# Performance work log

Hardware: AMD Instinct MI355X
Metric: run time of the kernel (lower is better)

## Reference

```python
import jax, jax.numpy as jnp
import numpy as np
import math

# ----- sizes -----
NUM_EDGES = 16384
NUM_NODES = 1024          # senders index into [0, NUM_NODES)
N_MUL = 64                # multiplicity n = V.shape[1]
AVG_NEIGH = 16.0          # avg_num_neighbors
F_IN = 64                 # scalar feature dim of x

# ----- real spherical harmonics (component normalization: sum_m Y_lm^2 = 2l+1) -----
_S3 = math.sqrt(3.0); _S5 = math.sqrt(5.0); _S15 = math.sqrt(15.0)
_C33 = math.sqrt(70.0)/4.0; _C32 = math.sqrt(105.0)/2.0
_C31 = math.sqrt(42.0)/4.0; _C30 = math.sqrt(7.0)/2.0; _CXYZ = math.sqrt(105.0)

def _sph(vn):
    x, y, z = vn[:, 0], vn[:, 1], vn[:, 2]
    Y0 = jnp.ones_like(x)[:, None]
    Y1 = _S3 * vn
    Y2 = jnp.stack([_S15*x*y, _S15*y*z, 0.5*_S5*(3*z*z - 1), _S15*x*z, 0.5*_S15*(x*x - y*y)], axis=1)
    Y3 = jnp.stack([_C33*y*(3*x*x - y*y), _CXYZ*x*y*z, _C31*y*(5*z*z - 1), _C30*z*(5*z*z - 3), _C31*x*(5*z*z - 1), _C32*z*(x*x - y*y), _C33*x*(x*x - 3*y*y)], axis=1)
    return [Y0, Y1, Y2, Y3]

# monomial form of the same SH, used to derive EXACT Clebsch-Gordan coefficients
_SHP = {
    0: [[(1.0, (0,0,0))]],
    1: [[(_S3, (1,0,0))], [(_S3, (0,1,0))], [(_S3, (0,0,1))]],
    2: [[(_S15, (1,1,0))], [(_S15, (0,1,1))], [(1.5*_S5, (0,0,2)), (-0.5*_S5, (0,0,0))], [(_S15, (1,0,1))], [(0.5*_S15, (2,0,0)), (-0.5*_S15, (0,2,0))]],
    3: [[(3*_C33, (2,1,0)), (-_C33, (0,3,0))], [(_CXYZ, (1,1,1))], [(5*_C31, (0,1,2)), (-_C31, (0,1,0))], [(5*_C30, (0,0,3)), (-3*_C30, (0,0,1))], [(5*_C31, (1,0,2)), (-_C31, (1,0,0))], [(_C32, (2,0,1)), (-_C32, (0,2,1))], [(_C33, (3,0,0)), (-3*_C33, (1,2,0))]],
}

def _dfact(n):
    r = 1
    while n > 1:
        r *= n; n -= 2
    return r

def _mono_int(e):
    # exact integral of x^a y^b z^c over the unit sphere
    a, b, c = e
    if (a % 2) or (b % 2) or (c % 2):
        return 0.0
    return 4.0*math.pi*_dfact(a-1)*_dfact(b-1)*_dfact(c-1)/_dfact(a+b+c+1)

def _pmul(p, q):
    return [(cp*cq, (a1+a2, b1+b2, c1+c2)) for cp, (a1,b1,c1) in p for cq, (a2,b2,c2) in q]

def _pint(p):
    return sum(c*_mono_int(e) for c, e in p)

def _cg(l1, l2, l3):
    # unique SO(3) intertwiner in this real-SH basis, scaled like e3nn component norm: sqrt(2l3+1)*w3j
    C = np.zeros((2*l1+1, 2*l2+1, 2*l3+1))
    for i, p1 in enumerate(_SHP[l1]):
        for j, p2 in enumerate(_SHP[l2]):
            p12 = _pmul(p1, p2)
            for k, p3 in enumerate(_SHP[l3]):
                C[i, j, k] = _pint(_pmul(p12, p3)) / (4.0*math.pi)
    return jnp.asarray(C / np.linalg.norm(C) * np.sqrt(2*l3+1), dtype=jnp.float32)

# tensor-product paths surviving filter_ir_out = 0e + 1o + 2e (inputs: SH 0e+1o+2e+3o, V 0e+1o+2e)
_PATHS0 = [(0,0), (1,1), (2,2)]
_PATHS1 = [(0,1), (1,0), (1,2), (2,1), (3,2)]
_PATHS2 = [(0,2), (1,1), (2,0), (2,2), (3,1)]
CGS = {(l1, l2, l3): _cg(l1, l2, l3) for l3, ps in ((0, _PATHS0), (1, _PATHS1), (2, _PATHS2)) for l1, l2 in ps}

# e3nn normalize_function(silu): divide by sqrt(E_{z~N(0,1)}[silu(z)^2])
_zg = np.linspace(-12.0, 12.0, 200001)
_phi = np.exp(-0.5*_zg*_zg)/np.sqrt(2.0*np.pi)
_sl = _zg/(1.0 + np.exp(-_zg))
ACT_C = float(np.sqrt(np.sum(_sl*_sl*_phi)*(_zg[1]-_zg[0])))

def _nsilu(v):
    return jax.nn.silu(v) / ACT_C

def _forward(vectors, x, V, senders, W_w, W1, W2, W3, Wv1, Wv2):
    E, n = V.shape[0], V.shape[1]
    d = jnp.linalg.norm(vectors, axis=1, keepdims=True)                 # [E,1] edge lengths
    vn = vectors / d
    Y = jnp.concatenate(_sph(vn), axis=1)                               # [E,16], ell = 0..3
    w = (x @ W_w) / math.sqrt(x.shape[1])                               # [E,n] edge weights (1-layer MLP, no act)
    wY = w[:, :, None] * Y[:, None, :]                                  # [E,n,16]
    agg = jax.ops.segment_sum(wY, senders, num_segments=NUM_NODES)[senders]  # scatter_sum + map_back
    agg = agg / math.sqrt(AVG_NEIGH)
    A = jnp.split(agg, [1, 4, 9], axis=2)                               # SH chunks: dims 1,3,5,7
    B = jnp.split(V, [1, 4], axis=2)                                    # V chunks: dims 1,3,5
    def tp(l1, l2, l3):
        return jnp.einsum('eni,enj,ijk->enk', A[l1], B[l2], CGS[(l1, l2, l3)])
    scal = jnp.concatenate([tp(a, b, 0) for a, b in _PATHS0], axis=2)   # [E,n,3] new scalars
    V1 = jnp.concatenate([tp(a, b, 1) for a, b in _PATHS1], axis=1)     # [E,5n,3] 1o paths
    V2 = jnp.concatenate([tp(a, b, 2) for a, b in _PATHS2], axis=1)     # [E,5n,5] 2e paths
    h = jnp.concatenate([x, scal.reshape(E, 3*n)], axis=1)              # [E, F_IN+3n]
    h = _nsilu(h @ W1 / math.sqrt(h.shape[1]))
    h = _nsilu(h @ W2 / math.sqrt(W2.shape[0]))
    h = h @ W3 / math.sqrt(W3.shape[0])                                 # output_activation=False
    # poly_envelope(p-1=5, 2), p=6: 1 - 28 d^6 + 48 d^7 - 21 d^8 on [0,1), 0 outside
    u = 1.0 - 28.0*d**6 + 48.0*d**7 - 21.0*d**8
    x_out = jnp.where(d < 1.0, u, 0.0) * h                              # [E,64]
    o1 = jnp.einsum('emi,mo->eoi', V1, Wv1) / math.sqrt(V1.shape[1])    # Linear per irrep: [E,n,3]
    o2 = jnp.einsum('emi,mo->eoi', V2, Wv2) / math.sqrt(V2.shape[1])    # [E,n,5]
    # output 0e block has no input path -> zeros (e3nn Linear, no bias)
    V_out = jnp.concatenate([jnp.zeros((E, n, 1), x_out.dtype), o1, o2], axis=2)  # [E,n,9]
    return x_out, V_out

def setup_inputs():
    key = jax.random.key(0)
    ks = jax.random.split(key, 10)
    E = NUM_EDGES
    vectors = 0.35 * jax.random.normal(ks[0], (E, 3), jnp.float32)   # mostly inside cutoff radius 1
    x = jax.random.normal(ks[1], (E, F_IN), jnp.float32)
    V = jax.random.normal(ks[2], (E, N_MUL, 9), jnp.float32)
    senders = jax.random.randint(ks[3], (E,), 0, NUM_NODES, dtype=jnp.int32)
    W_w = jax.random.normal(ks[4], (F_IN, N_MUL), jnp.float32)
    W1 = jax.random.normal(ks[5], (F_IN + 3*N_MUL, 64), jnp.float32)
    W2 = jax.random.normal(ks[6], (64, 64), jnp.float32)
    W3 = jax.random.normal(ks[7], (64, 64), jnp.float32)
    Wv1 = jax.random.normal(ks[8], (5*N_MUL, N_MUL), jnp.float32)
    Wv2 = jax.random.normal(ks[9], (5*N_MUL, N_MUL), jnp.float32)
    return {"vectors": vectors, "x": x, "V": V, "senders": senders, "W_w": W_w, "W1": W1, "W2": W2, "W3": W3, "Wv1": Wv1, "Wv2": Wv2}

def reference(vectors, x, V, senders, W_w, W1, W2, W3, Wv1, Wv2):
    return _forward(vectors, x, V, senders, W_w, W1, W2, W3, Wv1, Wv2)
```

## Files before the change

kernel.cpp:

```cpp
#include <hip/hip_runtime.h>
#include <math.h>

#define NNODES 1024
#define EDGES 16384
#define EB 4

typedef __attribute__((ext_vector_type(8))) short short8;
typedef __attribute__((ext_vector_type(4))) float f32x4;

__device__ __forceinline__ unsigned short f2bf(float f) {
  union { float f; unsigned int u; } v; v.f = f;
  unsigned int r = v.u + 0x7fffu + ((v.u >> 16) & 1u);
  return (unsigned short)(r >> 16);
}

__device__ __constant__ int PL1[13] = {0,1,2, 0,1,1,2,3, 0,1,2,2,3};
__device__ __constant__ int PL2[13] = {0,1,2, 1,0,2,1,2, 2,1,0,2,1};
__device__ __constant__ int PL3[13] = {0,0,0, 1,1,1,1,1, 2,2,2,2,2};
__device__ __constant__ int PCG[13] = {0,1,10, 35,44,53,98,143, 248,273,318,343,468};

__device__ __constant__ double SHC[16][2] = {
  {1.0, 0.0},
  {1.7320508075688772, 0.0},
  {1.7320508075688772, 0.0},
  {1.7320508075688772, 0.0},
  {3.8729833462074170, 0.0},
  {3.8729833462074170, 0.0},
  {3.3541019662496844, -1.1180339887498949},
  {3.8729833462074170, 0.0},
  {1.9364916731037085, -1.9364916731037085},
  {6.2749501990055667, -2.0916500663351889},
  {10.246950765959598, 0.0},
  {8.1009258730098255, -1.6201851746019651},
  {6.6143782776614768, -3.9686269665968861},
  {8.1009258730098255, -1.6201851746019651},
  {5.1234753829797990, -5.1234753829797990},
  {2.0916500663351889, -6.2749501990055667},
};
__device__ __constant__ int SHE[16][2] = {
  {0,0},{1,0},{16,0},{256,0},
  {17,0},{272,0},{512,0},{257,0},{2,32},
  {18,48},{273,0},{528,16},{768,256},{513,1},{258,288},{3,33}};

__global__ __launch_bounds__(256) void prep(
    const float* __restrict__ Wv1, const float* __restrict__ Wv2,
    const float* __restrict__ W1, const float* __restrict__ W2, const float* __restrict__ W3,
    unsigned short* __restrict__ wv1f, unsigned short* __restrict__ wv2f,
    unsigned short* __restrict__ w1f, unsigned short* __restrict__ w2f,
    unsigned short* __restrict__ w3f,
    float* __restrict__ cg, float* __restrict__ actp, int* __restrict__ counts)
{
  const int bid = blockIdx.x;
  const int t = threadIdx.x;

  if (bid < 13) {
    if (bid < 4) counts[bid*256 + t] = 0;
    __shared__ double sh[256];
    const int p = bid;
    const int LOFF[4] = {0,1,4,9};
    int l1 = PL1[p], l2 = PL2[p], l3 = PL3[p];
    int n1 = 2*l1+1, n2 = 2*l2+1, n3 = 2*l3+1;
    int nent = n1*n2*n3;
    const unsigned long long DP =
        1ULL | (1ULL<<7) | (1ULL<<14) | (2ULL<<21) | (3ULL<<28)
      | (8ULL<<35) | (15ULL<<42) | (48ULL<<49) | (105ULL<<56);
    double v = 0.0;
    if (t < nent) {
      int i = t / (n2*n3);
      int rem = t - i*(n2*n3);
      int j = rem / n3;
      int k = rem - j*n3;
      int lm1 = LOFF[l1]+i, lm2 = LOFF[l2]+j, lm3 = LOFF[l3]+k;
      double cs1[2] = {SHC[lm1][0], SHC[lm1][1]}; int es1[2] = {SHE[lm1][0], SHE[lm1][1]};
      double cs2[2] = {SHC[lm2][0], SHC[lm2][1]}; int es2[2] = {SHE[lm2][0], SHE[lm2][1]};
      double cs3[2] = {SHC[lm3][0], SHC[lm3][1]}; int es3[2] = {SHE[lm3][0], SHE[lm3][1]};
      #pragma unroll
      for (int t1 = 0; t1 < 2; t1++)
      #pragma unroll
      for (int t2 = 0; t2 < 2; t2++)
      #pragma unroll
      for (int t3 = 0; t3 < 2; t3++) {
        double cc = cs1[t1]*cs2[t2]*cs3[t3];
        int s = es1[t1] + es2[t2] + es3[t3];
        int a = s & 15, b = (s >> 4) & 15, c = (s >> 8) & 15;
        if (!((a|b|c) & 1)) {
          double num = (double)(int)((DP >> (7*a)) & 127)
                     * (double)(int)((DP >> (7*b)) & 127)
                     * (double)(int)((DP >> (7*c)) & 127);
          double den = (double)(int)((DP >> (7*(a+b+c+2))) & 127);
          v += cc * (num / den);
        }
      }
    }
    sh[t] = (t < nent) ? v*v : 0.0;
    __syncthreads();
    for (int d = 128; d > 0; d >>= 1) {
      if (t < d) sh[t] += sh[t+d];
      __syncthreads();
    }
    double scale = sqrt((double)(2*l3+1)) / sqrt(sh[0]);
    if (t < nent) cg[PCG[p] + t] = (float)(v * scale);

  } else if (bid < 21) {
    __shared__ float shf[256];
    const int b = bid - 13;
    const float dz = 24.0f / 200000.0f;
    float s = 0.f;
    for (int i = b*256 + t; i <= 200000; i += 8*256) {
      float z = -12.0f + dz * (float)i;
      float ph = __expf(-0.5f * z * z) * 0.3989422804014327f;
      float sl = z / (1.f + __expf(-z));
      s = fmaf(sl*sl, ph, s);
    }
    shf[t] = s;
    __syncthreads();
    for (int d = 128; d > 0; d >>= 1) {
      if (t < d) shf[t] += shf[t + d];
      __syncthreads();
    }
    if (t == 0) actp[b] = shf[0];

  } else {
    const int wid = t >> 6, lane = t & 63;
    const int g = (bid - 21)*4 + wid;
    const float* src; unsigned short* dst; int nk, f;
    if (g < 40)       { src = Wv1; dst = wv1f; nk = 10; f = g; }
    else if (g < 80)  { src = Wv2; dst = wv2f; nk = 10; f = g - 40; }
    else if (g < 112) { src = W1;  dst = w1f;  nk = 8;  f = g - 80; }
    else if (g < 120) { src = W2;  dst = w2f;  nk = 2;  f = g - 112; }
    else              { src = W3;  dst = w3f;  nk = 2;  f = g - 120; }
    int nt = f / nk;
    int ks = f - nt*nk;
    unsigned short us[8];
    #pragma unroll
    for (int j = 0; j < 8; j++) {
      float v = src[(ks*32 + (lane>>4)*8 + j)*64 + nt*16 + (lane & 15)];
      us[j] = f2bf(v);
    }
    uint4 pk;
    pk.x = (unsigned)us[0] | ((unsigned)us[1] << 16);
    pk.y = (unsigned)us[2] | ((unsigned)us[3] << 16);
    pk.z = (unsigned)us[4] | ((unsigned)us[5] << 16);
    pk.w = (unsigned)us[6] | ((unsigned)us[7] << 16);
    *(uint4*)(dst + ((size_t)f*64 + lane)*8) = pk;
  }
}

__global__ __launch_bounds__(256) void edgepass(
    const float* __restrict__ x, const float* __restrict__ Ww,
    const int* __restrict__ senders,
    float* __restrict__ w_ws, int* __restrict__ counts, int* __restrict__ elist, int E)
{
  const int wid = threadIdx.x >> 6, lane = threadIdx.x & 63;
  const int e = blockIdx.x * 4 + wid;
  if (e >= E) return;
  float xv = x[e*64 + lane];
  float w = 0.f;
  #pragma unroll
  for (int f = 0; f < 64; f++)
    w = fmaf(__shfl(xv, f), Ww[f*64 + lane], w);
  w_ws[e*64 + lane] = w * 0.125f;
  if (lane == 0) {
    int s = senders[e];
    int pos = atomicAdd(&counts[s], 1) & 63;
    elist[s*64 + pos] = e;
  }
}

__global__ __launch_bounds__(256) void k_node(
    const float* __restrict__ vec, const float* __restrict__ w_ws,
    const int* __restrict__ counts, const int* __restrict__ elist,
    float* __restrict__ node_agg)
{
  __shared__ float red[4*1024];
  const int wid = threadIdx.x >> 6, lane = threadIdx.x & 63;
  const int s = blockIdx.x;
  const int deg = min(counts[s], 64);

  const float S3 = 1.7320508075688772f, S5 = 2.23606797749979f, S15 = 3.872983346207417f;
  const float C33 = 2.091650066335189f, C32 = 5.123475382979799f, C31 = 1.6201851746019651f;
  const float C30 = 1.3228756555322954f, CX = 10.246950765959598f;

  float A[16];
  #pragma unroll
  for (int k = 0; k < 16; k++) A[k] = 0.f;

  for (int ii = wid; ii < deg; ii += 4) {
    int e = elist[s*64 + ii];
    float vx = vec[e*3+0], vy = vec[e*3+1], vz = vec[e*3+2];
    float d = sqrtf(vx*vx + vy*vy + vz*vz);
    float X = vx/d, Yv = vy/d, Z = vz/d;
    float y[16];
    y[0] = 1.f;
    y[1] = S3*X;  y[2] = S3*Yv;  y[3] = S3*Z;
    y[4] = S15*X*Yv; y[5] = S15*Yv*Z; y[6] = 0.5f*S5*(3.f*Z*Z - 1.f);
    y[7] = S15*X*Z;  y[8] = 0.5f*S15*(X*X - Yv*Yv);
    y[9]  = C33*Yv*(3.f*X*X - Yv*Yv);
    y[10] = CX*X*Yv*Z;
    y[11] = C31*Yv*(5.f*Z*Z - 1.f);
    y[12] = C30*Z*(5.f*Z*Z - 3.f);
    y[13] = C31*X*(5.f*Z*Z - 1.f);
    y[14] = C32*Z*(X*X - Yv*Yv);
    y[15] = C33*X*(X*X - 3.f*Yv*Yv);
    float wv = w_ws[e*64 + lane];
    #pragma unroll
    for (int k = 0; k < 16; k++) A[k] = fmaf(wv, y[k], A[k]);
  }
  #pragma unroll
  for (int k = 0; k < 16; k++) red[wid*1024 + lane*16 + k] = A[k];
  __syncthreads();
  const int t = threadIdx.x;
  f32x4 v0 = ((f32x4*)red)[t];
  f32x4 v1 = ((f32x4*)red)[256 + t];
  f32x4 v2 = ((f32x4*)red)[512 + t];
  f32x4 v3 = ((f32x4*)red)[768 + t];
  f32x4 sum = v0 + v1 + v2 + v3;
  ((f32x4*)(node_agg + (size_t)s*1024))[t] = sum;
}

template<int L1, int L2, int L3>
__device__ __forceinline__ void tp_path(const float* __restrict__ cgp,
    const float a[16], const float b[9], float o[2*L3+1])
{
  constexpr int N1 = 2*L1+1, N2 = 2*L2+1, N3 = 2*L3+1;
  constexpr int AO = (L1==0) ? 0 : (L1==1) ? 1 : (L1==2) ? 4 : 9;
  constexpr int BO = (L2==0) ? 0 : (L2==1) ? 1 : 4;
  constexpr int LM1 = (L1==0) ? 0 : (L1==1) ? 1 : (L1==2) ? 4 : 9;
  constexpr int LM2 = (L2==0) ? 0 : (L2==1) ? 1 : 4;
  constexpr int LM3 = (L3==0) ? 0 : (L3==1) ? 1 : 4;
  static constexpr unsigned char PAR[16] =
      {0, 1,2,4, 3,6,0,5,0, 2,7,2,4,1,4,1};
  #pragma unroll
  for (int k = 0; k < N3; k++) o[k] = 0.f;
  int ci = 0;
  #pragma unroll
  for (int i = 0; i < N1; i++) {
    #pragma unroll
    for (int j = 0; j < N2; j++) {
      float ab = a[AO+i] * b[BO+j];
      #pragma unroll
      for (int k = 0; k < N3; k++) {
        if ((PAR[LM1+i] ^ PAR[LM2+j] ^ PAR[LM3+k]) == 0)
          o[k] = fmaf(ab, cgp[ci], o[k]);
        ci++;
      }
    }
  }
}

__global__ __launch_bounds__(256, 4) void edge_main(
    const float* __restrict__ vec, const float* __restrict__ x,
    const float* __restrict__ V, const int* __restrict__ senders,
    const float* __restrict__ node_agg, const float* __restrict__ cg,
    const unsigned short* __restrict__ wv1f, const unsigned short* __restrict__ wv2f,
    const unsigned short* __restrict__ w1f, const unsigned short* __restrict__ w2f,
    const unsigned short* __restrict__ w3f,
    float* __restrict__ out, int E, const float* __restrict__ actp)
{
  __shared__ __align__(16) unsigned short V1sh[12*328];
  __shared__ __align__(16) unsigned short V2sh[20*328];
  __shared__ __align__(16) unsigned short zrow[336];
  __shared__ __align__(16) unsigned short hsh[4*264];
  __shared__ __align__(16) unsigned short h1sh[4*72];
  __shared__ __align__(16) unsigned short h2sh[4*72];
  __shared__ __align__(16) float vosh[4*584];
  __shared__ float ush[EB];

  const int t = threadIdx.x;
  const int wid = t >> 6, lane = t & 63;
  const int e0 = blockIdx.x * EB;
  const size_t E64 = (size_t)E * 64;
  const float inv_actc = 1.f / sqrtf((actp[0]+actp[1]+actp[2]+actp[3]
                                     +actp[4]+actp[5]+actp[6]+actp[7]) * (24.0f/200000.0f));

  if (t < 168) ((unsigned int*)zrow)[t] = 0u;

  { int el = t >> 6, o = t & 63;
    hsh[el*264 + o] = f2bf(x[(e0+el)*64 + o]); }

  {
    const int eloc = wid;
    const int eg = e0 + eloc;
    const int s = senders[eg];

    float a[16];
    const float* nap = node_agg + s*1024 + lane*16;
    #pragma unroll
    for (int k = 0; k < 16; k++) a[k] = nap[k] * 0.25f;

    float b[9];
    const float* vp = V + (size_t)eg*576 + lane*9;
    #pragma unroll
    for (int j = 0; j < 9; j++) b[j] = vp[j];

    float o1[1], o3[3], o5[5];
    tp_path<0,0,0>(cg + 0,  a, b, o1); hsh[eloc*264 + 64 + lane*3 + 0] = f2bf(o1[0]);
    tp_path<1,1,0>(cg + 1,  a, b, o1); hsh[eloc*264 + 64 + lane*3 + 1] = f2bf(o1[0]);
    tp_path<2,2,0>(cg + 10, a, b, o1); hsh[eloc*264 + 64 + lane*3 + 2] = f2bf(o1[0]);
    tp_path<0,1,1>(cg + 35, a, b, o3);
    { int r = eloc*3; for (int i=0;i<3;i++) V1sh[(r+i)*328 + 0*64 + lane] = f2bf(o3[i]); }
    tp_path<1,0,1>(cg + 44, a, b, o3);
    { int r = eloc*3; for (int i=0;i<3;i++) V1sh[(r+i)*328 + 1*64 + lane] = f2bf(o3[i]); }
    tp_path<1,2,1>(cg + 53, a, b, o3);
    { int r = eloc*3; for (int i=0;i<3;i++) V1sh[(r+i)*328 + 2*64 + lane] = f2bf(o3[i]); }
    tp_path<2,1,1>(cg + 98, a, b, o3);
    { int r = eloc*3; for (int i=0;i<3;i++) V1sh[(r+i)*328 + 3*64 + lane] = f2bf(o3[i]); }
    tp_path<3,2,1>(cg + 143, a, b, o3);
    { int r = eloc*3; for (int i=0;i<3;i++) V1sh[(r+i)*328 + 4*64 + lane] = f2bf(o3[i]); }
    tp_path<0,2,2>(cg + 248, a, b, o5);
    { int r = eloc*5; for (int i=0;i<5;i++) V2sh[(r+i)*328 + 0*64 + lane] = f2bf(o5[i]); }
    tp_path<1,1,2>(cg + 273, a, b, o5);
    { int r = eloc*5; for (int i=0;i<5;i++) V2sh[(r+i)*328 + 1*64 + lane] = f2bf(o5[i]); }
    tp_path<2,0,2>(cg + 318, a, b, o5);
    { int r = eloc*5; for (int i=0;i<5;i++) V2sh[(r+i)*328 + 2*64 + lane] = f2bf(o5[i]); }
    tp_path<2,2,2>(cg + 343, a, b, o5);
    { int r = eloc*5; for (int i=0;i<5;i++) V2sh[(r+i)*328 + 3*64 + lane] = f2bf(o5[i]); }
    tp_path<3,1,2>(cg + 468, a, b, o5);
    { int r = eloc*5; for (int i=0;i<5;i++) V2sh[(r+i)*328 + 4*64 + lane] = f2bf(o5[i]); }

    if (lane == 0) {
      float vx = vec[eg*3+0], vy = vec[eg*3+1], vz = vec[eg*3+2];
      float d = sqrtf(vx*vx + vy*vy + vz*vz);
      float u = 0.f;
      if (d < 1.f) {
        float d3 = d*d*d, d6 = d3*d3, d7 = d6*d, d8 = d7*d;
        u = 1.f - 28.f*d6 + 48.f*d7 - 21.f*d8;
      }
      ush[eloc] = u;
    }
  }
  __syncthreads();

  const int ntile = wid;
  const int qr = lane >> 4;
  const int ml = lane & 15;
  const float s320 = 0.05590169943749474f;

  {
    f32x4 acc = (f32x4){0,0,0,0};
    const unsigned short* p0 = (ml < 12) ? &V1sh[ml*328] : zrow;
    const unsigned short* bb = wv1f + ((size_t)(ntile*10)*64 + lane)*8;
    #pragma unroll
    for (int ks = 0; ks < 10; ks++) {
      short8 bf = *(const short8*)(bb + ks*512);
      short8 af = *(const short8*)(p0 + ks*32 + qr*8);
      acc = __builtin_amdgcn_mfma_f32_16x16x32_bf16(af, bf, acc, 0, 0, 0);
    }
    #pragma unroll
    for (int r = 0; r < 4; r++) {
      int row = qr*4 + r;
      if (row < 12) {
        int el = row / 3, i = row - (row/3)*3;
        vosh[el*584 + (ntile*16+ml)*9 + 1 + i] = acc[r] * s320;
      }
    }
  }

  {
    f32x4 acc[2]; acc[0] = (f32x4){0,0,0,0}; acc[1] = (f32x4){0,0,0,0};
    const unsigned short* p0 = &V2sh[ml*328];
    const unsigned short* p1 = (16+ml < 20) ? &V2sh[(16+ml)*328] : zrow;
    const unsigned short* bb = wv2f + ((size_t)(ntile*10)*64 + lane)*8;
    #pragma unroll
    for (int ks = 0; ks < 10; ks++) {
      short8 bf = *(const short8*)(bb + ks*512);
      int ao = ks*32 + qr*8;
      short8 af0 = *(const short8*)(p0 + ao);
      short8 af1 = *(const short8*)(p1 + ao);
      acc[0] = __builtin_amdgcn_mfma_f32_16x16x32_bf16(af0, bf, acc[0], 0, 0, 0);
      acc[1] = __builtin_amdgcn_mfma_f32_16x16x32_bf16(af1, bf, acc[1], 0, 0, 0);
    }
    #pragma unroll
    for (int mt = 0; mt < 2; mt++) {
      #pragma unroll
      for (int r = 0; r < 4; r++) {
        int row = mt*16 + qr*4 + r;
        if (row < 20) {
          int el = row / 5, i = row - (row/5)*5;
          vosh[el*584 + (ntile*16+ml)*9 + 4 + i] = acc[mt][r] * s320;
        }
      }
    }
  }

  { int el = t >> 6, o = t & 63;
    vosh[el*584 + o*9] = 0.f; }

  const unsigned short* hp = (ml < 4) ? &hsh[ml*264] : zrow;
  {
    f32x4 c = (f32x4){0,0,0,0};
    const unsigned short* bb = w1f + ((size_t)(ntile*8)*64 + lane)*8;
    #pragma unroll
    for (int ks = 0; ks < 8; ks++) {
      short8 bf = *(const short8*)(bb + ks*512);
      short8 af = *(const short8*)(hp + ks*32 + qr*8);
      c = __builtin_amdgcn_mfma_f32_16x16x32_bf16(af, bf, c, 0, 0, 0);
    }
    #pragma unroll
    for (int r = 0; r < 4; r++) {
      int row = qr*4 + r;
      if (row < 4) {
        float v = c[r] * 0.0625f;
        float sv = v / (1.f + expf(-v)) * inv_actc;
        h1sh[row*72 + ntile*16 + ml] = f2bf(sv);
      }
    }
  }
  __syncthreads();
  {
    f32x4 c = (f32x4){0,0,0,0};
    const unsigned short* ap = (ml < 4) ? &h1sh[ml*72] : zrow;
    const unsigned short* bb = w2f + ((size_t)(ntile*2)*64 + lane)*8;
    #pragma unroll
    for (int ks = 0; ks < 2; ks++) {
      short8 bf = *(const short8*)(bb + ks*512);
      short8 af = *(const short8*)(ap + ks*32 + qr*8);
      c = __builtin_amdgcn_mfma_f32_16x16x32_bf16(af, bf, c, 0, 0, 0);
    }
    #pragma unroll
    for (int r = 0; r < 4; r++) {
      int row = qr*4 + r;
      if (row < 4) {
        float v = c[r] * 0.125f;
        float sv = v / (1.f + expf(-v)) * inv_actc;
        h2sh[row*72 + ntile*16 + ml] = f2bf(sv);
      }
    }
  }
  __syncthreads();
  {
    f32x4 c = (f32x4){0,0,0,0};
    const unsigned short* ap = (ml < 4) ? &h2sh[ml*72] : zrow;
    const unsigned short* bb = w3f + ((size_t)(ntile*2)*64 + lane)*8;
    #pragma unroll
    for (int ks = 0; ks < 2; ks++) {
      short8 bf = *(const short8*)(bb + ks*512);
      short8 af = *(const short8*)(ap + ks*32 + qr*8);
      c = __builtin_amdgcn_mfma_f32_16x16x32_bf16(af, bf, c, 0, 0, 0);
    }
    #pragma unroll
    for (int r = 0; r < 4; r++) {
      int row = qr*4 + r;
      if (row < 4) {
        float v = c[r] * 0.125f;
        out[(size_t)(e0+row)*64 + ntile*16 + ml] = ush[row] * v;
      }
    }
  }

  for (int q = t; q < 576; q += 256) {
    int el = q / 144, i4 = q - (q/144)*144;
    ((f32x4*)(out + E64 + (size_t)(e0+el)*576))[i4] = ((f32x4*)(vosh + el*584))[i4];
  }
}

extern "C" void kernel_launch(void* const* d_in, const int* in_sizes, int n_in,
                              void* d_out, int out_size, void* d_ws, size_t ws_size,
                              hipStream_t stream)
{
  const float* vec     = (const float*)d_in[0];
  const float* x       = (const float*)d_in[1];
  const float* V       = (const float*)d_in[2];
  const int*   senders = (const int*)  d_in[3];
  const float* Ww      = (const float*)d_in[4];
  const float* W1      = (const float*)d_in[5];
  const float* W2      = (const float*)d_in[6];
  const float* W3      = (const float*)d_in[7];
  const float* Wv1     = (const float*)d_in[8];
  const float* Wv2     = (const float*)d_in[9];
  float* out = (float*)d_out;
  const int E = in_sizes[0] / 3;

  char* base = (char*)d_ws;
  float* node_agg = (float*)(base);
  float* w_ws     = (float*)(base + (4<<20));
  float* cg       = (float*)(base + (8<<20));
  float* actp     = (float*)(base + (8<<20) + 4096);
  int* counts     = (int*)  (base + (8<<20) + 8192);
  int* elist      = (int*)  (base + (8<<20) + 12288);
  unsigned short* wv1f = (unsigned short*)(base + (8<<20) + 278528);
  unsigned short* wv2f = (unsigned short*)(base + (8<<20) + 319488);
  unsigned short* w1f  = (unsigned short*)(base + (8<<20) + 360448);
  unsigned short* w2f  = (unsigned short*)(base + (8<<20) + 393216);
  unsigned short* w3f  = (unsigned short*)(base + (8<<20) + 401408);

  prep<<<53, 256, 0, stream>>>(Wv1, Wv2, W1, W2, W3,
                               wv1f, wv2f, w1f, w2f, w3f, cg, actp, counts);
  edgepass<<<(E+3)/4, 256, 0, stream>>>(x, Ww, senders, w_ws, counts, elist, E);
  k_node<<<NNODES, 256, 0, stream>>>(vec, w_ws, counts, elist, node_agg);
  edge_main<<<E/EB, 256, 0, stream>>>(vec, x, V, senders, node_agg, cg,
                                      wv1f, wv2f, w1f, w2f, w3f, out, E, actp);
}
```

Baseline: 169.1 us.

## Fuse edge weight matvec into node kernel, fold scales into weights, alias shared buffers

Removes the per-edge w_ws workspace by computing the x·Ww matvec inside k_node for each gathered edge. The senders bucketing moves into a lighter k_pre kernel that also converts weights to bf16. Normalisation scales (0.25 on CG, s320, 1/16, 1/8 and the activation constant) are folded into the precomputed CG and bf16 weights. In edge_main the V1/V2 and vosh shared buffers now alias each other and the occupancy hint rises from 4 to 6 blocks, with accumulator stores moved after the barrier. The x staging is vectorised. Folding scales before the bf16 rounding slightly changes numerics, and aliasing vosh over V12sh relies on the barrier ordering being correct.

```diff
diff --git a/kernel.cpp b/kernel.cpp
--- a/kernel.cpp
+++ b/kernel.cpp
@@ -2,7 +2,6 @@
 #include <math.h>
 
 #define NNODES 1024
-#define EDGES 16384
 #define EB 4
 
 typedef __attribute__((ext_vector_type(8))) short short8;
@@ -42,12 +41,7 @@
   {17,0},{272,0},{512,0},{257,0},{2,32},
   {18,48},{273,0},{528,16},{768,256},{513,1},{258,288},{3,33}};
 
-__global__ __launch_bounds__(256) void prep(
-    const float* __restrict__ Wv1, const float* __restrict__ Wv2,
-    const float* __restrict__ W1, const float* __restrict__ W2, const float* __restrict__ W3,
-    unsigned short* __restrict__ wv1f, unsigned short* __restrict__ wv2f,
-    unsigned short* __restrict__ w1f, unsigned short* __restrict__ w2f,
-    unsigned short* __restrict__ w3f,
+__global__ __launch_bounds__(256) void k_const(
     float* __restrict__ cg, float* __restrict__ actp, int* __restrict__ counts)
 {
   const int bid = blockIdx.x;
@@ -99,9 +93,9 @@
       __syncthreads();
     }
     double scale = sqrt((double)(2*l3+1)) / sqrt(sh[0]);
-    if (t < nent) cg[PCG[p] + t] = (float)(v * scale);
-
-  } else if (bid < 21) {
+    if (t < nent) cg[PCG[p] + t] = (float)(v * scale * 0.25);
+
+  } else {
     __shared__ float shf[256];
     const int b = bid - 13;
     const float dz = 24.0f / 200000.0f;
@@ -119,56 +113,59 @@
       __syncthreads();
     }
     if (t == 0) actp[b] = shf[0];
-
-  } else {
-    const int wid = t >> 6, lane = t & 63;
-    const int g = (bid - 21)*4 + wid;
-    const float* src; unsigned short* dst; int nk, f;
-    if (g < 40)       { src = Wv1; dst = wv1f; nk = 10; f = g; }
-    else if (g < 80)  { src = Wv2; dst = wv2f; nk = 10; f = g - 40; }
-    else if (g < 112) { src = W1;  dst = w1f;  nk = 8;  f = g - 80; }
-    else if (g < 120) { src = W2;  dst = w2f;  nk = 2;  f = g - 112; }
-    else              { src = W3;  dst = w3f;  nk = 2;  f = g - 120; }
-    int nt = f / nk;
-    int ks = f - nt*nk;
-    unsigned short us[8];
-    #pragma unroll
-    for (int j = 0; j < 8; j++) {
-      float v = src[(ks*32 + (lane>>4)*8 + j)*64 + nt*16 + (lane & 15)];
-      us[j] = f2bf(v);
-    }
-    uint4 pk;
-    pk.x = (unsigned)us[0] | ((unsigned)us[1] << 16);
-    pk.y = (unsigned)us[2] | ((unsigned)us[3] << 16);
-    pk.z = (unsigned)us[4] | ((unsigned)us[5] << 16);
-    pk.w = (unsigned)us[6] | ((unsigned)us[7] << 16);
-    *(uint4*)(dst + ((size_t)f*64 + lane)*8) = pk;
-  }
-}
-
-__global__ __launch_bounds__(256) void edgepass(
-    const float* __restrict__ x, const float* __restrict__ Ww,
-    const int* __restrict__ senders,
-    float* __restrict__ w_ws, int* __restrict__ counts, int* __restrict__ elist, int E)
+  }
+}
+
+__global__ __launch_bounds__(256) void k_pre(
+    const int* __restrict__ senders, int* __restrict__ counts, int* __restrict__ elist,
+    const float* __restrict__ Wv1, const float* __restrict__ Wv2,
+    const float* __restrict__ W1, const float* __restrict__ W2, const float* __restrict__ W3,
+    unsigned short* __restrict__ wv1f, unsigned short* __restrict__ wv2f,
+    unsigned short* __restrict__ w1f, unsigned short* __restrict__ w2f,
+    unsigned short* __restrict__ w3f,
+    const float* __restrict__ actp, int E)
 {
-  const int wid = threadIdx.x >> 6, lane = threadIdx.x & 63;
-  const int e = blockIdx.x * 4 + wid;
-  if (e >= E) return;
-  float xv = x[e*64 + lane];
-  float w = 0.f;
-  #pragma unroll
-  for (int f = 0; f < 64; f++)
-    w = fmaf(__shfl(xv, f), Ww[f*64 + lane], w);
-  w_ws[e*64 + lane] = w * 0.125f;
-  if (lane == 0) {
-    int s = senders[e];
-    int pos = atomicAdd(&counts[s], 1) & 63;
-    elist[s*64 + pos] = e;
-  }
+  const int t = threadIdx.x;
+  const int nsc = gridDim.x - 32;
+  if ((int)blockIdx.x < nsc) {
+    int e = blockIdx.x*256 + t;
+    if (e < E) {
+      int s = senders[e];
+      int pos = atomicAdd(&counts[s], 1) & 63;
+      elist[s*64 + pos] = e;
+    }
+    return;
+  }
+  const int wid = t >> 6, lane = t & 63;
+  const int g = (blockIdx.x - nsc)*4 + wid;
+  const float ia = rsqrtf((actp[0]+actp[1]+actp[2]+actp[3]
+                          +actp[4]+actp[5]+actp[6]+actp[7]) * (24.0f/200000.0f));
+  const float s320 = 0.05590169943749474f;
+  const float* src; unsigned short* dst; int nk, f; float sc;
+  if (g < 40)       { src = Wv1; dst = wv1f; nk = 10; f = g;       sc = s320; }
+  else if (g < 80)  { src = Wv2; dst = wv2f; nk = 10; f = g - 40;  sc = s320; }
+  else if (g < 112) { src = W1;  dst = w1f;  nk = 8;  f = g - 80;  sc = 0.0625f; }
+  else if (g < 120) { src = W2;  dst = w2f;  nk = 2;  f = g - 112; sc = 0.125f*ia; }
+  else              { src = W3;  dst = w3f;  nk = 2;  f = g - 120; sc = 0.125f*ia; }
+  int nt = f / nk;
+  int ks = f - nt*nk;
+  unsigned short us[8];
+  #pragma unroll
+  for (int j = 0; j < 8; j++) {
+    float v = src[(ks*32 + (lane>>4)*8 + j)*64 + nt*16 + (lane & 15)];
+    us[j] = f2bf(v * sc);
+  }
+  uint4 pk;
+  pk.x = (unsigned)us[0] | ((unsigned)us[1] << 16);
+  pk.y = (unsigned)us[2] | ((unsigned)us[3] << 16);
+  pk.z = (unsigned)us[4] | ((unsigned)us[5] << 16);
+  pk.w = (unsigned)us[6] | ((unsigned)us[7] << 16);
+  *(uint4*)(dst + ((size_t)f*64 + lane)*8) = pk;
 }
 
 __global__ __launch_bounds__(256) void k_node(
-    const float* __restrict__ vec, const float* __restrict__ w_ws,
+    const float* __restrict__ vec, const float* __restrict__ x,
+    const float* __restrict__ Ww,
     const int* __restrict__ counts, const int* __restrict__ elist,
     float* __restrict__ node_agg)
 {
@@ -187,6 +184,12 @@
 
   for (int ii = wid; ii < deg; ii += 4) {
     int e = elist[s*64 + ii];
+    float xv = x[(size_t)e*64 + lane];
+    float w = 0.f;
+    #pragma unroll
+    for (int f = 0; f < 64; f++)
+      w = fmaf(__shfl(xv, f), Ww[f*64 + lane], w);
+    w *= 0.125f;
     float vx = vec[e*3+0], vy = vec[e*3+1], vz = vec[e*3+2];
     float d = sqrtf(vx*vx + vy*vy + vz*vz);
     float X = vx/d, Yv = vy/d, Z = vz/d;
@@ -202,9 +205,8 @@
     y[13] = C31*X*(5.f*Z*Z - 1.f);
     y[14] = C32*Z*(X*X - Yv*Yv);
     y[15] = C33*X*(X*X - 3.f*Yv*Yv);
-    float wv = w_ws[e*64 + lane];
-    #pragma unroll
-    for (int k = 0; k < 16; k++) A[k] = fmaf(wv, y[k], A[k]);
+    #pragma unroll
+    for (int k = 0; k < 16; k++) A[k] = fmaf(w, y[k], A[k]);
   }
   #pragma unroll
   for (int k = 0; k < 16; k++) red[wid*1024 + lane*16 + k] = A[k];
@@ -248,50 +250,56 @@
   }
 }
 
-__global__ __launch_bounds__(256, 4) void edge_main(
+__global__ __launch_bounds__(256, 6) void edge_main(
     const float* __restrict__ vec, const float* __restrict__ x,
     const float* __restrict__ V, const int* __restrict__ senders,
     const float* __restrict__ node_agg, const float* __restrict__ cg,
     const unsigned short* __restrict__ wv1f, const unsigned short* __restrict__ wv2f,
     const unsigned short* __restrict__ w1f, const unsigned short* __restrict__ w2f,
     const unsigned short* __restrict__ w3f,
-    float* __restrict__ out, int E, const float* __restrict__ actp)
+    float* __restrict__ out, int E)
 {
-  __shared__ __align__(16) unsigned short V1sh[12*328];
-  __shared__ __align__(16) unsigned short V2sh[20*328];
+  __shared__ __align__(16) unsigned short V12sh[32*328];
   __shared__ __align__(16) unsigned short zrow[336];
   __shared__ __align__(16) unsigned short hsh[4*264];
   __shared__ __align__(16) unsigned short h1sh[4*72];
   __shared__ __align__(16) unsigned short h2sh[4*72];
-  __shared__ __align__(16) float vosh[4*584];
   __shared__ float ush[EB];
+
+  unsigned short* V1sh = V12sh;
+  unsigned short* V2sh = V12sh + 12*328;
+  float* vosh = (float*)V12sh;
 
   const int t = threadIdx.x;
   const int wid = t >> 6, lane = t & 63;
   const int e0 = blockIdx.x * EB;
   const size_t E64 = (size_t)E * 64;
-  const float inv_actc = 1.f / sqrtf((actp[0]+actp[1]+actp[2]+actp[3]
-                                     +actp[4]+actp[5]+actp[6]+actp[7]) * (24.0f/200000.0f));
 
   if (t < 168) ((unsigned int*)zrow)[t] = 0u;
 
-  { int el = t >> 6, o = t & 63;
-    hsh[el*264 + o] = f2bf(x[(e0+el)*64 + o]); }
+  if (t < 64) {
+    int el = t >> 4, off = (t & 15)*4;
+    f32x4 xv = *(const f32x4*)(x + (size_t)(e0 + el)*64 + off);
+    uint2 pk;
+    pk.x = (unsigned)f2bf(xv.x) | ((unsigned)f2bf(xv.y) << 16);
+    pk.y = (unsigned)f2bf(xv.z) | ((unsigned)f2bf(xv.w) << 16);
+    *(uint2*)(hsh + el*264 + off) = pk;
+  }
 
   {
     const int eloc = wid;
     const int eg = e0 + eloc;
+
+    float b[9];
+    const float* vp = V + (size_t)eg*576 + lane*9;
+    #pragma unroll
+    for (int j = 0; j < 9; j++) b[j] = vp[j];
+
     const int s = senders[eg];
-
     float a[16];
     const float* nap = node_agg + s*1024 + lane*16;
     #pragma unroll
-    for (int k = 0; k < 16; k++) a[k] = nap[k] * 0.25f;
-
-    float b[9];
-    const float* vp = V + (size_t)eg*576 + lane*9;
-    #pragma unroll
-    for (int j = 0; j < 9; j++) b[j] = vp[j];
+    for (int k = 0; k < 16; k++) a[k] = nap[k];
 
     float o1[1], o3[3], o5[5];
     tp_path<0,0,0>(cg + 0,  a, b, o1); hsh[eloc*264 + 64 + lane*3 + 0] = f2bf(o1[0]);
@@ -334,30 +342,21 @@
   const int ntile = wid;
   const int qr = lane >> 4;
   const int ml = lane & 15;
-  const float s320 = 0.05590169943749474f;
-
+
+  f32x4 acc1 = (f32x4){0,0,0,0};
   {
-    f32x4 acc = (f32x4){0,0,0,0};
     const unsigned short* p0 = (ml < 12) ? &V1sh[ml*328] : zrow;
     const unsigned short* bb = wv1f + ((size_t)(ntile*10)*64 + lane)*8;
     #pragma unroll
     for (int ks = 0; ks < 10; ks++) {
       short8 bf = *(const short8*)(bb + ks*512);
       short8 af = *(const short8*)(p0 + ks*32 + qr*8);
-      acc = __builtin_amdgcn_mfma_f32_16x16x32_bf16(af, bf, acc, 0, 0, 0);
-    }
-    #pragma unroll
-    for (int r = 0; r < 4; r++) {
-      int row = qr*4 + r;
-      if (row < 12) {
-        int el = row / 3, i = row - (row/3)*3;
-        vosh[el*584 + (ntile*16+ml)*9 + 1 + i] = acc[r] * s320;
-      }
-    }
-  }
-
+      acc1 = __builtin_amdgcn_mfma_f32_16x16x32_bf16(af, bf, acc1, 0, 0, 0);
+    }
+  }
+
+  f32x4 acc2a = (f32x4){0,0,0,0}, acc2b = (f32x4){0,0,0,0};
   {
-    f32x4 acc[2]; acc[0] = (f32x4){0,0,0,0}; acc[1] = (f32x4){0,0,0,0};
     const unsigned short* p0 = &V2sh[ml*328];
     const unsigned short* p1 = (16+ml < 20) ? &V2sh[(16+ml)*328] : zrow;
     const unsigned short* bb = wv2f + ((size_t)(ntile*10)*64 + lane)*8;
@@ -367,24 +366,10 @@
       int ao = ks*32 + qr*8;
       short8 af0 = *(const short8*)(p0 + ao);
       short8 af1 = *(const short8*)(p1 + ao);
-      acc[0] = __builtin_amdgcn_mfma_f32_16x16x32_bf16(af0, bf, acc[0], 0, 0, 0);
-      acc[1] = __builtin_amdgcn_mfma_f32_16x16x32_bf16(af1, bf, acc[1], 0, 0, 0);
-    }
-    #pragma unroll
-    for (int mt = 0; mt < 2; mt++) {
-      #pragma unroll
-      for (int r = 0; r < 4; r++) {
-        int row = mt*16 + qr*4 + r;
-        if (row < 20) {
-          int el = row / 5, i = row - (row/5)*5;
-          vosh[el*584 + (ntile*16+ml)*9 + 4 + i] = acc[mt][r] * s320;
-        }
-      }
-    }
-  }
-
-  { int el = t >> 6, o = t & 63;
-    vosh[el*584 + o*9] = 0.f; }
+      acc2a = __builtin_amdgcn_mfma_f32_16x16x32_bf16(af0, bf, acc2a, 0, 0, 0);
+      acc2b = __builtin_amdgcn_mfma_f32_16x16x32_bf16(af1, bf, acc2b, 0, 0, 0);
+    }
+  }
 
   const unsigned short* hp = (ml < 4) ? &hsh[ml*264] : zrow;
   {
@@ -400,13 +385,39 @@
     for (int r = 0; r < 4; r++) {
       int row = qr*4 + r;
       if (row < 4) {
-        float v = c[r] * 0.0625f;
-        float sv = v / (1.f + expf(-v)) * inv_actc;
+        float v = c[r];
+        float sv = v / (1.f + expf(-v));
         h1sh[row*72 + ntile*16 + ml] = f2bf(sv);
       }
     }
   }
   __syncthreads();
+
+  #pragma unroll
+  for (int r = 0; r < 4; r++) {
+    int row = qr*4 + r;
+    if (row < 12) {
+      int el = row / 3, i = row - (row/3)*3;
+      vosh[el*584 + (ntile*16+ml)*9 + 1 + i] = acc1[r];
+    }
+  }
+  #pragma unroll
+  for (int r = 0; r < 4; r++) {
+    int row = qr*4 + r;
+    int el = row / 5, i = row - (row/5)*5;
+    vosh[el*584 + (ntile*16+ml)*9 + 4 + i] = acc2a[r];
+  }
+  #pragma unroll
+  for (int r = 0; r < 4; r++) {
+    int row = 16 + qr*4 + r;
+    if (row < 20) {
+      int el = row / 5, i = row - (row/5)*5;
+      vosh[el*584 + (ntile*16+ml)*9 + 4 + i] = acc2b[r];
+    }
+  }
+  { int el = t >> 6, o = t & 63;
+    vosh[el*584 + o*9] = 0.f; }
+
   {
     f32x4 c = (f32x4){0,0,0,0};
     const unsigned short* ap = (ml < 4) ? &h1sh[ml*72] : zrow;
@@ -421,13 +432,14 @@
     for (int r = 0; r < 4; r++) {
       int row = qr*4 + r;
       if (row < 4) {
-        float v = c[r] * 0.125f;
-        float sv = v / (1.f + expf(-v)) * inv_actc;
+        float v = c[r];
+        float sv = v / (1.f + expf(-v));
         h2sh[row*72 + ntile*16 + ml] = f2bf(sv);
       }
     }
   }
   __syncthreads();
+
   {
     f32x4 c = (f32x4){0,0,0,0};
     const unsigned short* ap = (ml < 4) ? &h2sh[ml*72] : zrow;
@@ -442,8 +454,7 @@
     for (int r = 0; r < 4; r++) {
       int row = qr*4 + r;
       if (row < 4) {
-        float v = c[r] * 0.125f;
-        out[(size_t)(e0+row)*64 + ntile*16 + ml] = ush[row] * v;
+        out[(size_t)(e0+row)*64 + ntile*16 + ml] = ush[row] * c[r];
       }
     }
   }
@@ -473,8 +484,7 @@
 
   char* base = (char*)d_ws;
   float* node_agg = (float*)(base);
-  float* w_ws     = (float*)(base + (4<<20));
-  float* cg       = (float*)(base + (8<<20));
+  float* cgbuf    = (float*)(base + (8<<20));
   float* actp     = (float*)(base + (8<<20) + 4096);
   int* counts     = (int*)  (base + (8<<20) + 8192);
   int* elist      = (int*)  (base + (8<<20) + 12288);
@@ -484,10 +494,12 @@
   unsigned short* w2f  = (unsigned short*)(base + (8<<20) + 393216);
   unsigned short* w3f  = (unsigned short*)(base + (8<<20) + 401408);
 
-  prep<<<53, 256, 0, stream>>>(Wv1, Wv2, W1, W2, W3,
-                               wv1f, wv2f, w1f, w2f, w3f, cg, actp, counts);
-  edgepass<<<(E+3)/4, 256, 0, stream>>>(x, Ww, senders, w_ws, counts, elist, E);
-  k_node<<<NNODES, 256, 0, stream>>>(vec, w_ws, counts, elist, node_agg);
-  edge_main<<<E/EB, 256, 0, stream>>>(vec, x, V, senders, node_agg, cg,
-                                      wv1f, wv2f, w1f, w2f, w3f, out, E, actp);
-}
+  const int nsc = (E + 255) >> 8;
+  k_const<<<21, 256, 0, stream>>>(cgbuf, actp, counts);
+  k_pre<<<nsc + 32, 256, 0, stream>>>(senders, counts, elist,
+                                      Wv1, Wv2, W1, W2, W3,
+                                      wv1f, wv2f, w1f, w2f, w3f, actp, E);
+  k_node<<<NNODES, 256, 0, stream>>>(vec, x, Ww, counts, elist, node_agg);
+  edge_main<<<E/EB, 256, 0, stream>>>(vec, x, V, senders, node_agg, cgbuf,
+                                      wv1f, wv2f, w1f, w2f, w3f, out, E);
+}
```

New measurement: 178.0 us. 1.05x slower.
